# Optimization experiments

Hardware: AMD Instinct MI355X
Metric: run time of the kernel (lower is better)

The kernel has to match this reference:

```python
import jax, jax.numpy as jnp
import numpy as np

B, N, H = 4, 256, 256
BN_EPS = 1e-5
ETA_EPS = 1e-20


def setup_inputs() -> dict:
    key = jax.random.key(0)
    k1, k2, k3, k4 = jax.random.split(key, 4)
    scale = 1.0 / np.sqrt(H)
    return {
        "nodes_features": jax.random.normal(k1, (B, N, H), dtype=jnp.float32),
        "edges_features": jax.random.normal(k2, (B, N, N, H), dtype=jnp.float32),
        "W1": jax.random.normal(k3, (H, H), dtype=jnp.float32) * scale,
        "W2": jax.random.normal(k4, (H, H), dtype=jnp.float32) * scale,
        "gamma": jnp.ones((H,), dtype=jnp.float32),
        "beta": jnp.zeros((H,), dtype=jnp.float32),
    }


def reference(nodes_features, edges_features, W1, W2, gamma, beta):
    # Linear projections (nn.Linear: y = x @ W.T, no bias)
    x_left = jnp.einsum('bnh,oh->bno', nodes_features, W1)       # (B,N,H)
    x_w2 = jnp.einsum('bnh,oh->bno', nodes_features, W2)         # (B,N,H)

    # Edge gating: sigmoid-normalize over neighbor axis j (dim=2)
    sig = jax.nn.sigmoid(edges_features)                         # (B,N,N,H)
    eta = sig / (jnp.sum(sig, axis=2, keepdims=True) + ETA_EPS)  # (B,N,N,H)

    # Weighted aggregation: sum_j eta[b,i,j,h] * x_w2[b,j,h]
    right = jnp.einsum('bijh,bjh->bih', eta, x_w2)               # (B,N,H)

    equ = x_left + right                                         # (B,N,H)

    # BatchNorm1d over channel H with batch stats over (B, N) (training mode,
    # track_running_stats=False -> always uses batch statistics, biased var)
    mean = jnp.mean(equ, axis=(0, 1))                            # (H,)
    var = jnp.var(equ, axis=(0, 1))                              # (H,) biased
    normed = (equ - mean) * jax.lax.rsqrt(var + BN_EPS)
    return normed * gamma + beta
```

## Files before the change

### kernel.cpp

```cpp
#include <hip/hip_runtime.h>
#include <cstddef>

#define BB 4
#define NN 256
#define HH 256
#define BN_EPS 1e-5f
#define ETA_EPS 1e-20f

typedef float f4 __attribute__((ext_vector_type(4)));

__device__ __forceinline__ float fast_sigmoid(float x) {
    float ex = __expf(-x);
    return __builtin_amdgcn_rcpf(1.f + ex);
}

__global__ __launch_bounds__(256) void transpose_kernel(
    const float* __restrict__ W1, const float* __restrict__ W2,
    float* __restrict__ WT1, float* __restrict__ WT2)
{
    const int which = blockIdx.x >> 4;
    const int tile  = blockIdx.x & 15;
    const int tr = (tile >> 2) << 6, tc = (tile & 3) << 6;
    const float* __restrict__ W  = which ? W2 : W1;
    float* __restrict__ WT       = which ? WT2 : WT1;

    __shared__ float tl[64][65];
    const int c = threadIdx.x & 63, p0 = threadIdx.x >> 6;
#pragma unroll
    for (int p = 0; p < 16; ++p) {
        int r = p * 4 + p0;
        tl[c][r] = W[(tr + r) * HH + tc + c];
    }
    __syncthreads();
#pragma unroll
    for (int p = 0; p < 16; ++p) {
        int cc = p * 4 + p0;
        WT[(tc + cc) * HH + tr + c] = tl[cc][c];
    }
}

__global__ __launch_bounds__(256) void proj_kernel(
    const float* __restrict__ nodes, const float* __restrict__ WT1,
    const float* __restrict__ WT2, float* __restrict__ xleft,
    float* __restrict__ xw2)
{
    const int which = blockIdx.x >> 7;
    const int rb    = blockIdx.x & 127;
    const float* __restrict__ WT = which ? WT2 : WT1;
    float* __restrict__ out      = which ? xw2 : xleft;
    const int t = threadIdx.x;

    __shared__ float xs[8][HH];
    {
        f4* xs4 = reinterpret_cast<f4*>(xs);
        const f4* nodes4 = reinterpret_cast<const f4*>(nodes) + rb * 512;
#pragma unroll
        for (int m = 0; m < 2; ++m) xs4[m * 256 + t] = nodes4[m * 256 + t];
    }
    __syncthreads();

    const int oq = t & 63;
    const int hg = t >> 6;
    const f4* __restrict__ WT4 = reinterpret_cast<const f4*>(WT);

    f4 acc[8];
#pragma unroll
    for (int r = 0; r < 8; ++r) acc[r] = (f4){0.f, 0.f, 0.f, 0.f};

    for (int hh = 0; hh < 64; ++hh) {
        const int h = hg * 64 + hh;
        f4 wv = WT4[h * 64 + oq];
#pragma unroll
        for (int r = 0; r < 8; ++r)
            acc[r] += xs[r][h] * wv;
    }

    __shared__ f4 ps[4][8][64];
#pragma unroll
    for (int r = 0; r < 8; ++r) ps[hg][r][oq] = acc[r];
    __syncthreads();

#pragma unroll
    for (int m = 0; m < 2; ++m) {
        int idx = m * 256 + t;
        int r = idx >> 6, o = idx & 63;
        f4 v = ps[0][r][o] + ps[1][r][o] + ps[2][r][o] + ps[3][r][o];
        reinterpret_cast<f4*>(out)[(rb * 8 + r) * 64 + o] = v;
    }
}

__global__ __launch_bounds__(1024) void edge_kernel(
    const float* __restrict__ edges, const float* __restrict__ xw2,
    const float* __restrict__ xleft, float* __restrict__ equ)
{
    const int bi = blockIdx.x;
    const int b  = bi >> 8;
    const int t  = threadIdx.x;
    const int q  = t & 63;
    const int jg = t >> 6;

    const f4* __restrict__ e4 =
        reinterpret_cast<const f4*>(edges) + ((size_t)bi * NN + jg) * 64 + q;
    const f4* __restrict__ xw4 =
        reinterpret_cast<const f4*>(xw2) + ((size_t)b * NN + jg) * 64 + q;

    f4 s0 = (f4){0.f, 0.f, 0.f, 0.f};
    f4 s1 = (f4){0.f, 0.f, 0.f, 0.f};

#pragma unroll 4
    for (int jj = 0; jj < 16; ++jj) {
        f4 e  = __builtin_nontemporal_load(e4 + (size_t)jj * 16 * 64);
        f4 xw = xw4[(size_t)jj * 16 * 64];
#pragma unroll
        for (int k = 0; k < 4; ++k) {
            float sg = fast_sigmoid(e[k]);
            s0[k] += sg;
            s1[k] += sg * xw[k];
        }
    }

    __shared__ f4 red0[16][64];
    __shared__ f4 red1[16][64];
    red0[jg][q] = s0;
    red1[jg][q] = s1;
    __syncthreads();

    if (t < 64) {
        f4 S0 = (f4){0.f, 0.f, 0.f, 0.f};
        f4 S1 = (f4){0.f, 0.f, 0.f, 0.f};
#pragma unroll
        for (int g = 0; g < 16; ++g) { S0 += red0[g][t]; S1 += red1[g][t]; }
        f4 xl = reinterpret_cast<const f4*>(xleft)[bi * 64 + t];
        f4 o;
#pragma unroll
        for (int k = 0; k < 4; ++k) o[k] = xl[k] + S1[k] / (S0[k] + ETA_EPS);
        reinterpret_cast<f4*>(equ)[bi * 64 + t] = o;
    }
}

__global__ __launch_bounds__(1024) void statsnorm_kernel(
    const float* __restrict__ equ, const float* __restrict__ gamma,
    const float* __restrict__ beta, float* __restrict__ out)
{
    const int cq = blockIdx.x;
    const int t  = threadIdx.x;
    const int lane = t & 63, w = t >> 6;

    f4 v = reinterpret_cast<const f4*>(equ)[t * 64 + cq];
    f4 s = v;
    f4 qs = v * v;

#pragma unroll
    for (int off = 32; off >= 1; off >>= 1) {
#pragma unroll
        for (int k = 0; k < 4; ++k) {
            s[k]  += __shfl_xor(s[k], off);
            qs[k] += __shfl_xor(qs[k], off);
        }
    }

    __shared__ f4 ws_[16][2];
    if (lane == 0) { ws_[w][0] = s; ws_[w][1] = qs; }
    __syncthreads();

    __shared__ f4 sc_s, sh_s;
    if (t == 0) {
        f4 S = (f4){0.f, 0.f, 0.f, 0.f};
        f4 Q = (f4){0.f, 0.f, 0.f, 0.f};
#pragma unroll
        for (int g = 0; g < 16; ++g) { S += ws_[g][0]; Q += ws_[g][1]; }
        const float inv_n = 1.f / (float)(BB * NN);
        f4 gm = reinterpret_cast<const f4*>(gamma)[cq];
        f4 bt = reinterpret_cast<const f4*>(beta)[cq];
        f4 sc, sh;
#pragma unroll
        for (int k = 0; k < 4; ++k) {
            float mean = S[k] * inv_n;
            float var  = Q[k] * inv_n - mean * mean;
            float rstd = rsqrtf(var + BN_EPS);
            sc[k] = rstd * gm[k];
            sh[k] = bt[k] - mean * rstd * gm[k];
        }
        sc_s = sc; sh_s = sh;
    }
    __syncthreads();

    f4 sc = sc_s, sh = sh_s;
    f4 o;
#pragma unroll
    for (int k = 0; k < 4; ++k) o[k] = v[k] * sc[k] + sh[k];
    reinterpret_cast<f4*>(out)[t * 64 + cq] = o;
}

extern "C" void kernel_launch(void* const* d_in, const int* in_sizes, int n_in,
                              void* d_out, int out_size, void* d_ws, size_t ws_size,
                              hipStream_t stream) {
    (void)in_sizes; (void)n_in; (void)out_size; (void)ws_size;

    const float* nodes = (const float*)d_in[0];
    const float* edges = (const float*)d_in[1];
    const float* W1    = (const float*)d_in[2];
    const float* W2    = (const float*)d_in[3];
    const float* gamma = (const float*)d_in[4];
    const float* beta  = (const float*)d_in[5];
    float* out = (float*)d_out;

    const int nBN_H = BB * NN * HH;
    float* ws    = (float*)d_ws;
    float* xleft = ws;
    float* xw2   = ws + nBN_H;
    float* equ   = ws + 2 * nBN_H;
    float* WT1   = ws + 3 * nBN_H;
    float* WT2   = WT1 + HH * HH;

    transpose_kernel<<<32, 256, 0, stream>>>(W1, W2, WT1, WT2);
    proj_kernel<<<256, 256, 0, stream>>>(nodes, WT1, WT2, xleft, xw2);
    edge_kernel<<<BB * NN, 1024, 0, stream>>>(edges, xw2, xleft, equ);
    statsnorm_kernel<<<64, 1024, 0, stream>>>(equ, gamma, beta, out);
}
```

Before: 73.41 us.

## Split edge reduction over j into four blocks with partial-sum finish kernel

The edge kernel now uses 256-thread blocks, each handling a quarter of the neighbor axis for one (b,i) row, and each warp reads a contiguous run of 16 j rows instead of strided ones. Partial sums of sigmoid and weighted sigmoid go to a workspace buffer. A new finish kernel combines the four partials, divides, and adds xleft. The aim is finer-grained scheduling and better occupancy on the bandwidth-bound edge stream, at the cost of an extra launch and extra partial-sum traffic.

```diff
diff --git a/kernel.cpp b/kernel.cpp
--- a/kernel.cpp
+++ b/kernel.cpp
@@ -89,28 +89,31 @@
     }
 }
 
-__global__ __launch_bounds__(1024) void edge_kernel(
+__global__ __launch_bounds__(256, 8) void edge_kernel(
     const float* __restrict__ edges, const float* __restrict__ xw2,
-    const float* __restrict__ xleft, float* __restrict__ equ)
-{
-    const int bi = blockIdx.x;
-    const int b  = bi >> 8;
-    const int t  = threadIdx.x;
-    const int q  = t & 63;
-    const int jg = t >> 6;
+    f4* __restrict__ psum)
+{
+    const int blk = blockIdx.x;
+    const int bi  = blk >> 2;
+    const int jq  = blk & 3;
+    const int b   = bi >> 8;
+    const int t   = threadIdx.x;
+    const int q   = t & 63;
+    const int w   = t >> 6;
+    const int j0  = jq * 64 + w * 16;
 
     const f4* __restrict__ e4 =
-        reinterpret_cast<const f4*>(edges) + ((size_t)bi * NN + jg) * 64 + q;
+        reinterpret_cast<const f4*>(edges) + ((size_t)bi * NN + j0) * 64 + q;
     const f4* __restrict__ xw4 =
-        reinterpret_cast<const f4*>(xw2) + ((size_t)b * NN + jg) * 64 + q;
+        reinterpret_cast<const f4*>(xw2) + ((size_t)b * NN + j0) * 64 + q;
 
     f4 s0 = (f4){0.f, 0.f, 0.f, 0.f};
     f4 s1 = (f4){0.f, 0.f, 0.f, 0.f};
 
-#pragma unroll 4
+#pragma unroll 2
     for (int jj = 0; jj < 16; ++jj) {
-        f4 e  = __builtin_nontemporal_load(e4 + (size_t)jj * 16 * 64);
-        f4 xw = xw4[(size_t)jj * 16 * 64];
+        f4 e  = __builtin_nontemporal_load(e4 + jj * 64);
+        f4 xw = xw4[jj * 64];
 #pragma unroll
         for (int k = 0; k < 4; ++k) {
             float sg = fast_sigmoid(e[k]);
@@ -119,23 +122,39 @@
         }
     }
 
-    __shared__ f4 red0[16][64];
-    __shared__ f4 red1[16][64];
-    red0[jg][q] = s0;
-    red1[jg][q] = s1;
+    __shared__ f4 r0[4][64];
+    __shared__ f4 r1[4][64];
+    r0[w][q] = s0;
+    r1[w][q] = s1;
     __syncthreads();
 
     if (t < 64) {
-        f4 S0 = (f4){0.f, 0.f, 0.f, 0.f};
-        f4 S1 = (f4){0.f, 0.f, 0.f, 0.f};
-#pragma unroll
-        for (int g = 0; g < 16; ++g) { S0 += red0[g][t]; S1 += red1[g][t]; }
-        f4 xl = reinterpret_cast<const f4*>(xleft)[bi * 64 + t];
-        f4 o;
-#pragma unroll
-        for (int k = 0; k < 4; ++k) o[k] = xl[k] + S1[k] / (S0[k] + ETA_EPS);
-        reinterpret_cast<f4*>(equ)[bi * 64 + t] = o;
-    }
+        f4 S0 = r0[0][t] + r0[1][t] + r0[2][t] + r0[3][t];
+        f4 S1 = r1[0][t] + r1[1][t] + r1[2][t] + r1[3][t];
+        f4* p = psum + (((size_t)jq * 1024 + bi) * 64 + t) * 2;
+        p[0] = S0;
+        p[1] = S1;
+    }
+}
+
+__global__ __launch_bounds__(256) void finish_kernel(
+    const f4* __restrict__ psum, const float* __restrict__ xleft,
+    float* __restrict__ equ)
+{
+    const int idx = blockIdx.x * 256 + threadIdx.x;
+    f4 S0 = (f4){0.f, 0.f, 0.f, 0.f};
+    f4 S1 = (f4){0.f, 0.f, 0.f, 0.f};
+#pragma unroll
+    for (int jq = 0; jq < 4; ++jq) {
+        const f4* p = psum + ((size_t)jq * 65536 + idx) * 2;
+        S0 += p[0];
+        S1 += p[1];
+    }
+    f4 xl = reinterpret_cast<const f4*>(xleft)[idx];
+    f4 o;
+#pragma unroll
+    for (int k = 0; k < 4; ++k) o[k] = xl[k] + S1[k] / (S0[k] + ETA_EPS);
+    reinterpret_cast<f4*>(equ)[idx] = o;
 }
 
 __global__ __launch_bounds__(1024) void statsnorm_kernel(
@@ -212,9 +231,11 @@
     float* equ   = ws + 2 * nBN_H;
     float* WT1   = ws + 3 * nBN_H;
     float* WT2   = WT1 + HH * HH;
+    f4*    psum  = (f4*)(WT2 + HH * HH);
 
     transpose_kernel<<<32, 256, 0, stream>>>(W1, W2, WT1, WT2);
     proj_kernel<<<256, 256, 0, stream>>>(nodes, WT1, WT2, xleft, xw2);
-    edge_kernel<<<BB * NN, 1024, 0, stream>>>(edges, xw2, xleft, equ);
+    edge_kernel<<<BB * NN * 4, 256, 0, stream>>>(edges, xw2, psum);
+    finish_kernel<<<256, 256, 0, stream>>>(psum, xleft, equ);
     statsnorm_kernel<<<64, 1024, 0, stream>>>(equ, gamma, beta, out);
 }
```

Result: slower. 80.04 us (+9.0%).

## Retile edge kernel to share staged xw2 across 8 rows per block

Applied to the files above, without the earlier changes.

Each edge block now covers 8 consecutive (b,i) rows and a 64-channel slice instead of one row with all channels. The matching xw2 slice is staged once in shared memory and reused across the 8 rows, which cuts repeated global/L2 reads of xw2. The cost is a smaller grid (512 blocks), extra syncs, a shared-memory reduction that reuses the staging buffer, and 64-byte contiguous edge segments per row instead of full 1 KB rows, which may hurt coalescing of the dominant edge stream.

```diff
diff --git a/kernel.cpp b/kernel.cpp
--- a/kernel.cpp
+++ b/kernel.cpp
@@ -93,24 +93,40 @@
     const float* __restrict__ edges, const float* __restrict__ xw2,
     const float* __restrict__ xleft, float* __restrict__ equ)
 {
-    const int bi = blockIdx.x;
-    const int b  = bi >> 8;
-    const int t  = threadIdx.x;
-    const int q  = t & 63;
-    const int jg = t >> 6;
-
-    const f4* __restrict__ e4 =
-        reinterpret_cast<const f4*>(edges) + ((size_t)bi * NN + jg) * 64 + q;
+    const int blk = blockIdx.x;
+    const int ig  = blk >> 2;
+    const int hs4 = (blk & 3) * 16;
+    const int bi0 = ig * 8;
+    const int b   = bi0 >> 8;
+    const int t   = threadIdx.x;
+
+    __shared__ f4 xw_s[NN][16];
+
     const f4* __restrict__ xw4 =
-        reinterpret_cast<const f4*>(xw2) + ((size_t)b * NN + jg) * 64 + q;
-
-    f4 s0 = (f4){0.f, 0.f, 0.f, 0.f};
-    f4 s1 = (f4){0.f, 0.f, 0.f, 0.f};
-
-#pragma unroll 4
-    for (int jj = 0; jj < 16; ++jj) {
-        f4 e  = __builtin_nontemporal_load(e4 + (size_t)jj * 16 * 64);
-        f4 xw = xw4[(size_t)jj * 16 * 64];
+        reinterpret_cast<const f4*>(xw2) + (size_t)b * NN * 64;
+#pragma unroll
+    for (int m = 0; m < 4; ++m) {
+        int idx = m * 1024 + t;
+        int j = idx >> 4, q = idx & 15;
+        xw_s[j][q] = xw4[j * 64 + hs4 + q];
+    }
+    __syncthreads();
+
+    const int q  = t & 15;
+    const int il = (t >> 4) & 7;
+    const int jg = t >> 7;
+
+    const f4* __restrict__ erow =
+        reinterpret_cast<const f4*>(edges) +
+        (size_t)(bi0 + il) * (NN * 64) + hs4 + q;
+
+    float s0[4] = {0.f, 0.f, 0.f, 0.f};
+    float s1[4] = {0.f, 0.f, 0.f, 0.f};
+
+#pragma unroll 2
+    for (int j = jg; j < NN; j += 8) {
+        f4 e  = __builtin_nontemporal_load(erow + j * 64);
+        f4 xw = xw_s[j][q];
 #pragma unroll
         for (int k = 0; k < 4; ++k) {
             float sg = fast_sigmoid(e[k]);
@@ -118,23 +134,28 @@
             s1[k] += sg * xw[k];
         }
     }
-
-    __shared__ f4 red0[16][64];
-    __shared__ f4 red1[16][64];
-    red0[jg][q] = s0;
-    red1[jg][q] = s1;
-    __syncthreads();
-
-    if (t < 64) {
-        f4 S0 = (f4){0.f, 0.f, 0.f, 0.f};
-        f4 S1 = (f4){0.f, 0.f, 0.f, 0.f};
-#pragma unroll
-        for (int g = 0; g < 16; ++g) { S0 += red0[g][t]; S1 += red1[g][t]; }
-        f4 xl = reinterpret_cast<const f4*>(xleft)[bi * 64 + t];
-        f4 o;
-#pragma unroll
-        for (int k = 0; k < 4; ++k) o[k] = xl[k] + S1[k] / (S0[k] + ETA_EPS);
-        reinterpret_cast<f4*>(equ)[bi * 64 + t] = o;
+    __syncthreads();
+
+    float* red = reinterpret_cast<float*>(xw_s);
+    {
+        float* r0 = red + ((jg * 8 + il) * 16 + q) * 4;
+        float* r1 = r0 + 4096;
+#pragma unroll
+        for (int k = 0; k < 4; ++k) { r0[k] = s0[k]; r1[k] = s1[k]; }
+    }
+    __syncthreads();
+
+    if (t < 512) {
+        const int il2 = t >> 6;
+        const int ch  = t & 63;
+        float S0 = 0.f, S1 = 0.f;
+#pragma unroll
+        for (int g = 0; g < 8; ++g) {
+            S0 += red[(g * 8 + il2) * 64 + ch];
+            S1 += red[(g * 8 + il2) * 64 + ch + 4096];
+        }
+        const size_t off = (size_t)(bi0 + il2) * HH + hs4 * 4 + ch;
+        equ[off] = xleft[off] + S1 / (S0 + ETA_EPS);
     }
 }
 
@@ -215,6 +236,6 @@
 
     transpose_kernel<<<32, 256, 0, stream>>>(W1, W2, WT1, WT2);
     proj_kernel<<<256, 256, 0, stream>>>(nodes, WT1, WT2, xleft, xw2);
-    edge_kernel<<<BB * NN, 1024, 0, stream>>>(edges, xw2, xleft, equ);
+    edge_kernel<<<512, 1024, 0, stream>>>(edges, xw2, xleft, equ);
     statsnorm_kernel<<<64, 1024, 0, stream>>>(equ, gamma, beta, out);
 }
```

Result: no change. 73.98 us (+0.8%).
